# Performance work log

Hardware: AMD Instinct MI355X
Metric: run time of the kernel (lower is better)

Reference implementation:

```python
import jax, jax.numpy as jnp
import numpy as np

B, N, M = 2048, 4096, 4096


def setup_inputs() -> dict:
    key = jax.random.key(0)
    kt, kv, kr = jax.random.split(key, 3)
    # sorted abscissae per sample (interp1d assumes monotone t)
    t = jnp.sort(jax.random.uniform(kt, (B, N), dtype=jnp.float32), axis=-1)
    v = jax.random.normal(kv, (B, N), dtype=jnp.float32)
    # queries slightly outside [0,1] to exercise the extrapolation clamp
    r = jax.random.uniform(kr, (B, M), minval=-0.05, maxval=1.05, dtype=jnp.float32)
    return {"t": t, "v": v, "r": r}


def _interp1(t, v, r):
    # t: [N] sorted, v: [N], r: [M]
    idx = jnp.clip(jnp.searchsorted(t, r, side='right'), 1, t.shape[0] - 1)
    t0 = t[idx - 1]
    t1 = t[idx]
    v0 = v[idx - 1]
    v1 = v[idx]
    denom = jnp.where(t1 == t0, jnp.float32(1.0), t1 - t0)
    out = v0 + (r - t0) / denom * (v1 - v0)
    # scipy fill_value=(v[0], v[-1]) with bounds_error=False: clamp extrapolation
    out = jnp.where(r < t[0], v[0], out)
    out = jnp.where(r > t[-1], v[-1], out)
    return out


def reference(t, v, r):
    # batched 1D linear interpolation with clamped extrapolation -> [B, M]
    return jax.vmap(_interp1)(t, v, r)
```

## Files before the change

### kernel.cpp

```cpp
#include <hip/hip_runtime.h>

constexpr int B = 2048;
constexpr int N = 4096;
constexpr int M = 4096;
constexpr int K = 2048;
constexpr int T = 512;

__global__ __launch_bounds__(T, 8) void interp_kernel(
    const float* __restrict__ t,
    const float* __restrict__ v,
    const float* __restrict__ r,
    float* __restrict__ out) {
    __shared__ float2 stv[N];
    __shared__ int lut[K];

    const int b = blockIdx.x;
    const float* tb = t + (size_t)b * N;
    const float* vb = v + (size_t)b * N;
    const float* rb = r + (size_t)b * M;
    float* ob = out + (size_t)b * M;

    for (int i = threadIdx.x; i < N / 4; i += T) {
        const float4 t4 = ((const float4*)tb)[i];
        const float4 v4 = ((const float4*)vb)[i];
        stv[4 * i + 0] = make_float2(t4.x, v4.x);
        stv[4 * i + 1] = make_float2(t4.y, v4.y);
        stv[4 * i + 2] = make_float2(t4.z, v4.z);
        stv[4 * i + 3] = make_float2(t4.w, v4.w);
    }
    for (int k = threadIdx.x; k < K; k += T) lut[k] = N;
    __syncthreads();

    for (int j = threadIdx.x; j < N; j += T) {
        const float tj = stv[j].x;
        int khi = (int)(tj * K);
        if (khi > K - 1) khi = K - 1;
        int klo = 0;
        if (j > 0) klo = (int)(stv[j - 1].x * K) + 1;
        for (int k = klo; k <= khi; ++k) lut[k] = j;
    }
    __syncthreads();

    const float tfirst = stv[0].x;
    const float vfirst = stv[0].y;
    const float tlast = stv[N - 1].x;
    const float vlast = stv[N - 1].y;

    const float4* r4 = (const float4*)rb;
    float4* o4 = (float4*)ob;
    const int ia = threadIdx.x;
    const int ib = ia + T;
    const float4 qa = r4[ia];
    const float4 qb = r4[ib];
    float q[8] = {qa.x, qa.y, qa.z, qa.w, qb.x, qb.y, qb.z, qb.w};
    int lo[8];

    #pragma unroll
    for (int j = 0; j < 8; ++j) {
        int k = (int)(q[j] * K);
        k = k < 0 ? 0 : (k > K - 1 ? K - 1 : k);
        lo[j] = lut[k];
    }
    #pragma unroll
    for (int j = 0; j < 8; ++j) {
        #pragma unroll
        for (int s = 0; s < 3; ++s) {
            const int safe = lo[j] < N - 1 ? lo[j] : N - 1;
            lo[j] += (stv[safe].x <= q[j]) ? 1 : 0;
        }
        while (lo[j] < N && stv[lo[j]].x <= q[j]) ++lo[j];
    }
    float o[8];
    #pragma unroll
    for (int j = 0; j < 8; ++j) {
        const int idx = lo[j] < 1 ? 1 : (lo[j] > N - 1 ? N - 1 : lo[j]);
        const float2 p0 = stv[idx - 1];
        const float2 p1 = stv[idx];
        const float d = p1.x - p0.x;
        const float rden = __builtin_amdgcn_rcpf(d == 0.0f ? 1.0f : d);
        float oo = p0.y + (q[j] - p0.x) * rden * (p1.y - p0.y);
        oo = (q[j] < tfirst) ? vfirst : oo;
        oo = (q[j] > tlast) ? vlast : oo;
        o[j] = oo;
    }
    o4[ia] = make_float4(o[0], o[1], o[2], o[3]);
    o4[ib] = make_float4(o[4], o[5], o[6], o[7]);
}

extern "C" void kernel_launch(void* const* d_in, const int* in_sizes, int n_in,
                              void* d_out, int out_size, void* d_ws, size_t ws_size,
                              hipStream_t stream) {
    const float* t = (const float*)d_in[0];
    const float* v = (const float*)d_in[1];
    const float* r = (const float*)d_in[2];
    float* out = (float*)d_out;
    interp_kernel<<<B, T, 0, stream>>>(t, v, r, out);
}
```

Measured before the change: 140.8 us.

## Split t/v shared arrays, use sentinel-padded search and denser 16-bit LUT

Splits the interleaved float2 shared array into separate t and v arrays so the global-to-shared copy is a straight float4 store. It pads t with FLT_MAX sentinels so the linear search needs no bounds checks. It also roughly doubles the bucket LUT resolution while storing it as unsigned short, which keeps shared memory in check and shortens the search steps. Query loads are hoisted before the staging loop to overlap their latency. The trade-offs are more LUT fill work per block and two separate shared loads for t and v in the interpolation step.

Result: faster. 135.7 us (-3.6%).

```diff
diff --git a/kernel.cpp b/kernel.cpp
--- a/kernel.cpp
+++ b/kernel.cpp
@@ -1,9 +1,10 @@
 #include <hip/hip_runtime.h>
+#include <float.h>
 
 constexpr int B = 2048;
 constexpr int N = 4096;
 constexpr int M = 4096;
-constexpr int K = 2048;
+constexpr int K = 4088;
 constexpr int T = 512;
 
 __global__ __launch_bounds__(T, 8) void interp_kernel(
@@ -11,8 +12,9 @@
     const float* __restrict__ v,
     const float* __restrict__ r,
     float* __restrict__ out) {
-    __shared__ float2 stv[N];
-    __shared__ int lut[K];
+    __shared__ __align__(16) float st[N + 4];
+    __shared__ __align__(16) float sv[N];
+    __shared__ unsigned short lut[K];
 
     const int b = blockIdx.x;
     const float* tb = t + (size_t)b * N;
@@ -20,69 +22,65 @@
     const float* rb = r + (size_t)b * M;
     float* ob = out + (size_t)b * M;
 
-    for (int i = threadIdx.x; i < N / 4; i += T) {
-        const float4 t4 = ((const float4*)tb)[i];
-        const float4 v4 = ((const float4*)vb)[i];
-        stv[4 * i + 0] = make_float2(t4.x, v4.x);
-        stv[4 * i + 1] = make_float2(t4.y, v4.y);
-        stv[4 * i + 2] = make_float2(t4.z, v4.z);
-        stv[4 * i + 3] = make_float2(t4.w, v4.w);
-    }
-    for (int k = threadIdx.x; k < K; k += T) lut[k] = N;
-    __syncthreads();
-
-    for (int j = threadIdx.x; j < N; j += T) {
-        const float tj = stv[j].x;
-        int khi = (int)(tj * K);
-        if (khi > K - 1) khi = K - 1;
-        int klo = 0;
-        if (j > 0) klo = (int)(stv[j - 1].x * K) + 1;
-        for (int k = klo; k <= khi; ++k) lut[k] = j;
-    }
-    __syncthreads();
-
-    const float tfirst = stv[0].x;
-    const float vfirst = stv[0].y;
-    const float tlast = stv[N - 1].x;
-    const float vlast = stv[N - 1].y;
-
     const float4* r4 = (const float4*)rb;
-    float4* o4 = (float4*)ob;
     const int ia = threadIdx.x;
     const int ib = ia + T;
     const float4 qa = r4[ia];
     const float4 qb = r4[ib];
+
+    for (int i = threadIdx.x; i < N / 4; i += T) {
+        ((float4*)st)[i] = ((const float4*)tb)[i];
+        ((float4*)sv)[i] = ((const float4*)vb)[i];
+    }
+    if (threadIdx.x == 0) { st[N] = FLT_MAX; st[N + 1] = FLT_MAX; }
+    for (int k = threadIdx.x; k < K; k += T) lut[k] = (unsigned short)N;
+    __syncthreads();
+
+    for (int j = threadIdx.x; j < N; j += T) {
+        const float tj = st[j];
+        int khi = (int)(tj * (float)K);
+        if (khi > K - 1) khi = K - 1;
+        const int klo = (j > 0) ? (int)(st[j - 1] * (float)K) + 1 : 0;
+        for (int k = klo; k <= khi; ++k) lut[k] = (unsigned short)j;
+    }
+    __syncthreads();
+
+    const float tfirst = st[0];
+    const float vfirst = sv[0];
+    const float tlast = st[N - 1];
+    const float vlast = sv[N - 1];
+
     float q[8] = {qa.x, qa.y, qa.z, qa.w, qb.x, qb.y, qb.z, qb.w};
     int lo[8];
 
     #pragma unroll
     for (int j = 0; j < 8; ++j) {
-        int k = (int)(q[j] * K);
+        int k = (int)(q[j] * (float)K);
         k = k < 0 ? 0 : (k > K - 1 ? K - 1 : k);
         lo[j] = lut[k];
     }
     #pragma unroll
     for (int j = 0; j < 8; ++j) {
-        #pragma unroll
-        for (int s = 0; s < 3; ++s) {
-            const int safe = lo[j] < N - 1 ? lo[j] : N - 1;
-            lo[j] += (stv[safe].x <= q[j]) ? 1 : 0;
-        }
-        while (lo[j] < N && stv[lo[j]].x <= q[j]) ++lo[j];
+        lo[j] += (st[lo[j]] <= q[j]) ? 1 : 0;
+        lo[j] += (st[lo[j]] <= q[j]) ? 1 : 0;
+        while (st[lo[j]] <= q[j]) ++lo[j];
     }
     float o[8];
     #pragma unroll
     for (int j = 0; j < 8; ++j) {
         const int idx = lo[j] < 1 ? 1 : (lo[j] > N - 1 ? N - 1 : lo[j]);
-        const float2 p0 = stv[idx - 1];
-        const float2 p1 = stv[idx];
-        const float d = p1.x - p0.x;
+        const float t0 = st[idx - 1];
+        const float t1 = st[idx];
+        const float v0 = sv[idx - 1];
+        const float v1 = sv[idx];
+        const float d = t1 - t0;
         const float rden = __builtin_amdgcn_rcpf(d == 0.0f ? 1.0f : d);
-        float oo = p0.y + (q[j] - p0.x) * rden * (p1.y - p0.y);
+        float oo = v0 + (q[j] - t0) * rden * (v1 - v0);
         oo = (q[j] < tfirst) ? vfirst : oo;
         oo = (q[j] > tlast) ? vlast : oo;
         o[j] = oo;
     }
+    float4* o4 = (float4*)ob;
     o4[ia] = make_float4(o[0], o[1], o[2], o[3]);
     o4[ib] = make_float4(o[4], o[5], o[6], o[7]);
 }
```
